# Kernel tuning notes

Hardware: AMD Instinct MI355X
Metric: run time of the kernel (lower is better)

Reference implementation:

```python
import jax, jax.numpy as jnp
import numpy as np

SEARCH_RANGE = 4  # matches args.search_range


def _displacements(r):
    # Exact channel ordering of the original double loop:
    # I=0 -> (0,0); then for i=1..r: (-i,0),(+i,0),(0,-i),(0,+i),
    # then for j=1..r: (-i,-j),(+i,+j),(-i,+j),(+i,-j).
    ds = [(0, 0)]
    for i in range(1, r + 1):
        ds += [(-i, 0), (i, 0), (0, -i), (0, i)]
        for j in range(1, r + 1):
            ds += [(-i, -j), (i, j), (-i, j), (i, -j)]
    return ds


def setup_inputs() -> dict:
    key = jax.random.key(0)
    k1, k2 = jax.random.split(key)
    B, C, H, W = 4, 128, 96, 160
    src = jax.random.normal(k1, (B, C, H, W), dtype=jnp.float32)
    tgt = jax.random.normal(k2, (B, C, H, W), dtype=jnp.float32)
    return {"src": src, "tgt": tgt}


def reference(src, tgt):
    r = SEARCH_RANGE
    B, C, H, W = src.shape
    D = (2 * r + 1) ** 2  # 81 displacement channels
    # Zero-pad tgt spatially so out-of-range shifted regions contribute 0,
    # matching the torch version's zero-initialized output slices.
    tgt_pad = jnp.pad(tgt, ((0, 0), (0, 0), (r, r), (r, r)))
    chans = []
    for dy, dx in _displacements(r):
        # shifted[b,c,y,x] = tgt[b,c,y+dy,x+dx] (0 outside)
        t = jax.lax.dynamic_slice(tgt_pad, (0, 0, r + dy, r + dx), (B, C, H, W))
        chans.append(jnp.einsum('bchw,bchw->bhw', src, t))
    out = jnp.stack(chans, axis=1)  # [B, D, H, W]
    return out / D
```

## Files before the change

kernel.cpp:

```cpp
#include <hip/hip_runtime.h>
#include <hip/hip_bf16.h>

#define BATCH 4
#define CHAN 128
#define HGT 96
#define WID 160
#define HW (HGT * WID)
#define THREADS 512

typedef __attribute__((ext_vector_type(8))) short short8;
typedef __attribute__((ext_vector_type(4))) float float4v;

__device__ __forceinline__ int chan_of(int dy, int dx) {
    if (dy == 0 && dx == 0) return 0;
    if (dx == 0) { int i = dy < 0 ? -dy : dy; return 1 + (i - 1) * 20 + (dy < 0 ? 0 : 1); }
    if (dy == 0) { int i = dx < 0 ? -dx : dx; return 1 + (i - 1) * 20 + (dx < 0 ? 2 : 3); }
    int i = dy < 0 ? -dy : dy;
    int j = dx < 0 ? -dx : dx;
    int s = (dy < 0) ? (dx < 0 ? 0 : 2) : (dx < 0 ? 3 : 1);
    return 1 + (i - 1) * 20 + 4 + (j - 1) * 4 + s;
}

__device__ __forceinline__ unsigned pk2(float a, float b) {
    __hip_bfloat162 h = __float22bfloat162_rn(make_float2(a, b));
    unsigned u;
    __builtin_memcpy(&u, &h, 4);
    return u;
}

union sl_u { uint4 v; short8 s; };

#define FST_DECODE(TAG, U)                                                    \
    const int u##TAG   = (U);                                                 \
    const int xq##TAG  = u##TAG % 6;                                          \
    const int r6##TAG  = u##TAG / 6;                              \
    const int oct##TAG = r6##TAG & 15;                                        \
    const int row##TAG = r6##TAG >> 4;                             \
    const int gr##TAG  = y0 - 4 + row##TAG;                                   \
    const int gx##TAG  = x0 - 4 + xq##TAG * 4;               \
    const bool ok##TAG = ((unsigned)gr##TAG < (unsigned)HGT) &&               \
                         ((unsigned)gx##TAG < (unsigned)WID);                 \
    const int ga##TAG  = tb + (oct##TAG * 8 * HGT + gr##TAG) * WID + gx##TAG;

#define FST_ISSUE(TAG, COND)                                                  \
    _Pragma("unroll")                                                         \
    for (int j = 0; j < 8; ++j)                                               \
        p##TAG[j] = (COND) ? *(const float4v*)(tgt + ga##TAG + j * HW)        \
                           : (float4v){0.f, 0.f, 0.f, 0.f};

#define FST_WRITE(TAG)                                                        \
    _Pragma("unroll")                                                         \
    for (int i = 0; i < 4; ++i) {                                             \
        const int xl = xq##TAG * 4 + i;                                       \
        uint4 val;                                                            \
        val.x = pk2(p##TAG[0][i], p##TAG[1][i]);                              \
        val.y = pk2(p##TAG[2][i], p##TAG[3][i]);                              \
        val.z = pk2(p##TAG[4][i], p##TAG[5][i]);                              \
        val.w = pk2(p##TAG[6][i], p##TAG[7][i]);                              \
        s_b[(row##TAG * 24 + xl) * 16 + (oct##TAG ^ (xl & 15))] = val;        \
    }

#define COMPUTE_DY(DD, DYI)                                                   \
    {                                                                         \
        const int rr = wvy + (DYI);                                           \
        float4v a0 = (float4v){0.f, 0.f, 0.f, 0.f};                           \
        float4v a1 = (float4v){0.f, 0.f, 0.f, 0.f};                           \
        _Pragma("unroll")                                                     \
        for (int ks = 0; ks < 4; ++ks) {                                      \
            sl_u b0;                                        \
            b0.v = s_b[(rr * 24 + ln) * 16 + ((q + ks * 4) ^ ln)];            \
            a0 = __builtin_amdgcn_mfma_f32_16x16x32_bf16(afr[ks], b0.s, a0, 0, 0, 0); \
        }                                                                     \
        _Pragma("unroll")                                                     \
        for (int ks = 0; ks < 4; ++ks) {                                      \
            sl_u b1;                                     \
            b1.v = s_b[(rr * 24 + 16 + ln) * 16 + ((q + ks * 4) ^ ln)];       \
            a1 = __builtin_amdgcn_mfma_f32_16x16x32_bf16(afr[ks], b1.s, a1, 0, 0, 0); \
        }                                                                     \
        aa0[DD] = a0; aa1[DD] = a1;                                           \
    }

#define EPI_DY(DD, DYI)                                                       \
    _Pragma("unroll")                                                         \
    for (int reg = 0; reg < 4; ++reg) {                                       \
        const int m = q * 4 + reg;                                            \
        const int t0x = ln - m;                            \
        if ((unsigned)t0x <= 8u)                                              \
            s_o[((DYI) * 9 + t0x) * 68 + wvy * 16 + m] = aa0[DD][reg] * inv;  \
        const int t1x = ln + 16 - m;                       \
        if ((unsigned)t1x <= 8u)                                              \
            s_o[((DYI) * 9 + t1x) * 68 + wvy * 16 + m] = aa1[DD][reg] * inv;  \
    }

__global__ __launch_bounds__(THREADS, 4)
void cost_volume_fused(const float* __restrict__ src,
                       const float* __restrict__ tgt,
                       float* __restrict__ out) {
    __shared__ __align__(16) uint4 s_b[4736];
    __shared__ int s_tab[81];

    const int tid  = threadIdx.x;
    const int wv   = tid >> 6;
    const int wvy  = wv & 3;
    const int wvd  = wv >> 2;
    const int lane = tid & 63;
    const int q    = lane >> 4;
    const int ln   = lane & 15;

    const int w    = blockIdx.x;
    const int slab = w & 7;
    const int b    = slab >> 1;
    const int yh   = slab & 1;
    const int t    = w >> 3;
    const int x0   = (t % 10) * 16;
    const int y0   = yh * 48 + (t / 10) * 4;

    if (tid < 81) s_tab[tid] = chan_of(tid / 9 - 4, tid % 9 - 4) * HW;

    const int tb = b * CHAN * HGT * WID;

    FST_DECODE(0, tid)
    FST_DECODE(1, tid + 512)
    FST_DECODE(2, tid + 1024)
    const bool has2 = tid < 128;

    float4v p0[8], p1[8], p2[8];

    FST_ISSUE(0, ok0)

    const int y = y0 + wvy;
    const int sbase = (b * CHAN * HGT + y) * WID + x0 + ln + q * 8 * HW;
    float apay[32];
    #pragma unroll
    for (int ks = 0; ks < 4; ++ks)
        #pragma unroll
        for (int j = 0; j < 8; ++j)
            apay[ks * 8 + j] = src[sbase + (ks * 32 + j) * HW];

    FST_ISSUE(1, ok1)
    FST_WRITE(0)
    FST_ISSUE(2, has2 && ok2)
    short8 afr[4];
    #pragma unroll
    for (int ks = 0; ks < 4; ++ks) {
        sl_u f;
        f.v.x = pk2(apay[ks * 8 + 0], apay[ks * 8 + 1]);
        f.v.y = pk2(apay[ks * 8 + 2], apay[ks * 8 + 3]);
        f.v.z = pk2(apay[ks * 8 + 4], apay[ks * 8 + 5]);
        f.v.w = pk2(apay[ks * 8 + 6], apay[ks * 8 + 7]);
        afr[ks] = f.s;
    }
    FST_WRITE(1)
    if (has2) { FST_WRITE(2) }

    __syncthreads();

    float4v aa0[5], aa1[5];
    if (wvd == 0) {
        #pragma unroll
        for (int dd = 0; dd < 4; ++dd) COMPUTE_DY(dd, dd)
    } else {
        #pragma unroll
        for (int dd = 0; dd < 5; ++dd) COMPUTE_DY(dd, dd + 4)
    }

    __syncthreads();

    float* s_o = (float*)s_b;
    const float inv = 1.0f / 81.0f;
    if (wvd == 0) {
        #pragma unroll
        for (int dd = 0; dd < 4; ++dd) EPI_DY(dd, dd)
    } else {
        #pragma unroll
        for (int dd = 0; dd < 5; ++dd) EPI_DY(dd, dd + 4)
    }
    __syncthreads();

    const size_t ob = (size_t)b * 81 * HW + (size_t)y0 * WID + x0;
    #pragma unroll
    for (int it = 0; it < 3; ++it) {
        const int v = it * THREADS + tid;
        if (v < 1296) {
            const int xq  = v & 3;
            const int row = v >> 2;
            const int cix = row >> 2;
            const int yy  = row & 3;
            float4v val = *(const float4v*)&s_o[cix * 68 + yy * 16 + xq * 4];
            *(float4v*)&out[ob + s_tab[cix] + yy * WID + xq * 4] = val;
        }
    }
}

extern "C" void kernel_launch(void* const* d_in, const int* in_sizes, int n_in,
                              void* d_out, int out_size, void* d_ws, size_t ws_size,
                              hipStream_t stream) {
    const float* src = (const float*)d_in[0];
    const float* tgt = (const float*)d_in[1];
    float* out = (float*)d_out;
    cost_volume_fused<<<dim3(960, 1, 1), dim3(THREADS, 1, 1), 0, stream>>>(src, tgt, out);
}
```

Measured before the change: 116.7 us.

## Pre-convert inputs to NHWC bf16 in a separate pass and load via LDS DMA

Adds a prepass kernel that transposes src and tgt from NCHW fp32 into NHWC bf16 in the workspace. The main MFMA kernel then loads tgt tiles straight into LDS with global_load_lds and reads src fragments as contiguous 16-byte vectors. This removes the strided per-channel fp32 loads and the in-register bf16 packing from the main kernel. In exchange it adds a second kernel launch and a full extra read and write of both inputs. The old fused kernel remains as a fallback when the workspace is too small.

```diff
diff --git a/kernel.cpp b/kernel.cpp
--- a/kernel.cpp
+++ b/kernel.cpp
@@ -7,6 +7,8 @@
 #define WID 160
 #define HW (HGT * WID)
 #define THREADS 512
+#define TENSOR_ELEMS (BATCH * CHAN * HGT * WID)
+#define WS_NEED ((size_t)(2 * (size_t)TENSOR_ELEMS * 2))
 
 typedef __attribute__((ext_vector_type(8))) short short8;
 typedef __attribute__((ext_vector_type(4))) float float4v;
@@ -30,14 +32,178 @@
 
 union sl_u { uint4 v; short8 s; };
 
+__global__ __launch_bounds__(256)
+void nhwc_bf16_kernel(const float* __restrict__ src,
+                      const float* __restrict__ tgt,
+                      ushort* __restrict__ ws) {
+    __shared__ unsigned s_t[64][65];
+    int r = blockIdx.x;
+    const int xb = r % 3; r /= 3;
+    const int y  = r % HGT; r /= HGT;
+    const int b  = r % BATCH; r /= BATCH;
+    const float* in = r ? tgt : src;
+    ushort* op0 = ws + (size_t)r * TENSOR_ELEMS;
+    const int x0 = xb * 64;
+    const int npx = (x0 + 64 <= WID) ? 64 : (WID - x0);
+
+    const int t  = threadIdx.x;
+    const int x1 = t & 63, cp0 = t >> 6;
+    if (x1 < npx) {
+        const int base = (b * CHAN * HGT + y) * WID + x0 + x1;
+        #pragma unroll
+        for (int i = 0; i < 16; ++i) {
+            const int cp = cp0 + i * 4;
+            s_t[cp][x1] = pk2(in[base + (2 * cp) * HW],
+                              in[base + (2 * cp + 1) * HW]);
+        }
+    }
+    __syncthreads();
+    const int x2 = t >> 2, g = t & 3;
+    if (x2 < npx) {
+        ushort* op = op0 + ((size_t)(b * HGT + y) * WID + x0 + x2) * CHAN + g * 32;
+        #pragma unroll
+        for (int k = 0; k < 4; ++k) {
+            uint4 v;
+            v.x = s_t[g * 16 + k * 4 + 0][x2];
+            v.y = s_t[g * 16 + k * 4 + 1][x2];
+            v.z = s_t[g * 16 + k * 4 + 2][x2];
+            v.w = s_t[g * 16 + k * 4 + 3][x2];
+            *(uint4*)(op + k * 8) = v;
+        }
+    }
+}
+
+__global__ __launch_bounds__(THREADS, 4)
+void cost_volume_mfma(const ushort* __restrict__ srcT,
+                      const ushort* __restrict__ tgtT,
+                      float* __restrict__ out) {
+    __shared__ __align__(16) uint4 s_b[4736];
+    __shared__ int s_tab[81];
+
+    const int tid  = threadIdx.x;
+    const int wv   = tid >> 6;
+    const int wvy  = wv & 3;
+    const int wvd  = wv >> 2;
+    const int lane = tid & 63;
+    const int q    = lane >> 4;
+    const int ln   = lane & 15;
+
+    const int w    = blockIdx.x;
+    const int slab = w & 7;
+    const int b    = slab >> 1;
+    const int yh   = slab & 1;
+    const int t    = w >> 3;
+    const int x0   = (t % 10) * 16;
+    const int y0   = yh * 48 + (t / 10) * 4;
+
+    if (tid < 81) s_tab[tid] = chan_of(tid / 9 - 4, tid % 9 - 4) * HW;
+
+    const ushort* tbase = tgtT + (size_t)b * HGT * WID * CHAN;
+    #pragma unroll
+    for (int k = 0; k < 9; ++k) {
+        const int u   = k * THREADS + tid;
+        const int j   = u & 15;
+        const int v16 = u >> 4;
+        const int row = v16 / 24;
+        const int x   = v16 - row * 24;
+        const int gr  = y0 - 4 + row;
+        const int gx  = x0 - 4 + x;
+        const int oct = j ^ (x & 15);
+        unsigned* lp = (unsigned*)&s_b[k * THREADS + (tid & ~63)];
+        if (((unsigned)gr < (unsigned)HGT) && ((unsigned)gx < (unsigned)WID)) {
+            const unsigned* gp =
+                (const unsigned*)(tbase + ((gr * WID + gx) * CHAN + oct * 8));
+            __builtin_amdgcn_global_load_lds(gp, lp, 16, 0, 0);
+        } else {
+            s_b[u] = make_uint4(0u, 0u, 0u, 0u);
+        }
+    }
+
+    const int y = y0 + wvy;
+    const ushort* abase =
+        srcT + ((size_t)(b * HGT + y) * WID + x0 + ln) * CHAN + q * 8;
+    short8 afr[4];
+    #pragma unroll
+    for (int ks = 0; ks < 4; ++ks)
+        afr[ks] = *(const short8*)(abase + ks * 32);
+
+    __syncthreads();
+
+    float4v aa0[5], aa1[5];
+    #define COMPUTE_DY(DD, DYI)                                               \
+        {                                                                     \
+            const int rr = wvy + (DYI);                                       \
+            float4v a0 = (float4v){0.f, 0.f, 0.f, 0.f};                       \
+            float4v a1 = (float4v){0.f, 0.f, 0.f, 0.f};                       \
+            _Pragma("unroll")                                                 \
+            for (int ks = 0; ks < 4; ++ks) {                                  \
+                sl_u b0;                                    \
+                b0.v = s_b[(rr * 24 + ln) * 16 + ((q + ks * 4) ^ ln)];        \
+                a0 = __builtin_amdgcn_mfma_f32_16x16x32_bf16(afr[ks], b0.s, a0, 0, 0, 0); \
+            }                                                                 \
+            _Pragma("unroll")                                                 \
+            for (int ks = 0; ks < 4; ++ks) {                                  \
+                sl_u b1;                                 \
+                b1.v = s_b[(rr * 24 + 16 + ln) * 16 + ((q + ks * 4) ^ ln)];   \
+                a1 = __builtin_amdgcn_mfma_f32_16x16x32_bf16(afr[ks], b1.s, a1, 0, 0, 0); \
+            }                                                                 \
+            aa0[DD] = a0; aa1[DD] = a1;                                       \
+        }
+    if (wvd == 0) {
+        #pragma unroll
+        for (int dd = 0; dd < 4; ++dd) COMPUTE_DY(dd, dd)
+    } else {
+        #pragma unroll
+        for (int dd = 0; dd < 5; ++dd) COMPUTE_DY(dd, dd + 4)
+    }
+
+    __syncthreads();
+
+    float* s_o = (float*)s_b;
+    const float inv = 1.0f / 81.0f;
+    #define EPI_DY(DD, DYI)                                                   \
+        _Pragma("unroll")                                                     \
+        for (int reg = 0; reg < 4; ++reg) {                                   \
+            const int m = q * 4 + reg;                                        \
+            const int t0x = ln - m;                        \
+            if ((unsigned)t0x <= 8u)                                          \
+                s_o[((DYI) * 9 + t0x) * 68 + wvy * 16 + m] = aa0[DD][reg] * inv; \
+            const int t1x = ln + 16 - m;                   \
+            if ((unsigned)t1x <= 8u)                                          \
+                s_o[((DYI) * 9 + t1x) * 68 + wvy * 16 + m] = aa1[DD][reg] * inv; \
+        }
+    if (wvd == 0) {
+        #pragma unroll
+        for (int dd = 0; dd < 4; ++dd) EPI_DY(dd, dd)
+    } else {
+        #pragma unroll
+        for (int dd = 0; dd < 5; ++dd) EPI_DY(dd, dd + 4)
+    }
+    __syncthreads();
+
+    const size_t ob = (size_t)b * 81 * HW + (size_t)y0 * WID + x0;
+    #pragma unroll
+    for (int it = 0; it < 3; ++it) {
+        const int v = it * THREADS + tid;
+        if (v < 1296) {
+            const int xq  = v & 3;
+            const int row = v >> 2;
+            const int cix = row >> 2;
+            const int yy  = row & 3;
+            float4v val = *(const float4v*)&s_o[cix * 68 + yy * 16 + xq * 4];
+            *(float4v*)&out[ob + s_tab[cix] + yy * WID + xq * 4] = val;
+        }
+    }
+}
+
 #define FST_DECODE(TAG, U)                                                    \
     const int u##TAG   = (U);                                                 \
     const int xq##TAG  = u##TAG % 6;                                          \
-    const int r6##TAG  = u##TAG / 6;                              \
+    const int r6##TAG  = u##TAG / 6;                                          \
     const int oct##TAG = r6##TAG & 15;                                        \
-    const int row##TAG = r6##TAG >> 4;                             \
+    const int row##TAG = r6##TAG >> 4;                                        \
     const int gr##TAG  = y0 - 4 + row##TAG;                                   \
-    const int gx##TAG  = x0 - 4 + xq##TAG * 4;               \
+    const int gx##TAG  = x0 - 4 + xq##TAG * 4;                                \
     const bool ok##TAG = ((unsigned)gr##TAG < (unsigned)HGT) &&               \
                          ((unsigned)gx##TAG < (unsigned)WID);                 \
     const int ga##TAG  = tb + (oct##TAG * 8 * HGT + gr##TAG) * WID + gx##TAG;
@@ -60,38 +226,6 @@
         s_b[(row##TAG * 24 + xl) * 16 + (oct##TAG ^ (xl & 15))] = val;        \
     }
 
-#define COMPUTE_DY(DD, DYI)                                                   \
-    {                                                                         \
-        const int rr = wvy + (DYI);                                           \
-        float4v a0 = (float4v){0.f, 0.f, 0.f, 0.f};                           \
-        float4v a1 = (float4v){0.f, 0.f, 0.f, 0.f};                           \
-        _Pragma("unroll")                                                     \
-        for (int ks = 0; ks < 4; ++ks) {                                      \
-            sl_u b0;                                        \
-            b0.v = s_b[(rr * 24 + ln) * 16 + ((q + ks * 4) ^ ln)];            \
-            a0 = __builtin_amdgcn_mfma_f32_16x16x32_bf16(afr[ks], b0.s, a0, 0, 0, 0); \
-        }                                                                     \
-        _Pragma("unroll")                                                     \
-        for (int ks = 0; ks < 4; ++ks) {                                      \
-            sl_u b1;                                     \
-            b1.v = s_b[(rr * 24 + 16 + ln) * 16 + ((q + ks * 4) ^ ln)];       \
-            a1 = __builtin_amdgcn_mfma_f32_16x16x32_bf16(afr[ks], b1.s, a1, 0, 0, 0); \
-        }                                                                     \
-        aa0[DD] = a0; aa1[DD] = a1;                                           \
-    }
-
-#define EPI_DY(DD, DYI)                                                       \
-    _Pragma("unroll")                                                         \
-    for (int reg = 0; reg < 4; ++reg) {                                       \
-        const int m = q * 4 + reg;                                            \
-        const int t0x = ln - m;                            \
-        if ((unsigned)t0x <= 8u)                                              \
-            s_o[((DYI) * 9 + t0x) * 68 + wvy * 16 + m] = aa0[DD][reg] * inv;  \
-        const int t1x = ln + 16 - m;                       \
-        if ((unsigned)t1x <= 8u)                                              \
-            s_o[((DYI) * 9 + t1x) * 68 + wvy * 16 + m] = aa1[DD][reg] * inv;  \
-    }
-
 __global__ __launch_bounds__(THREADS, 4)
 void cost_volume_fused(const float* __restrict__ src,
                        const float* __restrict__ tgt,
@@ -125,7 +259,6 @@
     const bool has2 = tid < 128;
 
     float4v p0[8], p1[8], p2[8];
-
     FST_ISSUE(0, ok0)
 
     const int y = y0 + wvy;
@@ -198,5 +331,12 @@
     const float* src = (const float*)d_in[0];
     const float* tgt = (const float*)d_in[1];
     float* out = (float*)d_out;
-    cost_volume_fused<<<dim3(960, 1, 1), dim3(THREADS, 1, 1), 0, stream>>>(src, tgt, out);
-}
+    if (d_ws && ws_size >= WS_NEED) {
+        ushort* ws = (ushort*)d_ws;
+        nhwc_bf16_kernel<<<dim3(2304, 1, 1), dim3(256, 1, 1), 0, stream>>>(src, tgt, ws);
+        cost_volume_mfma<<<dim3(960, 1, 1), dim3(THREADS, 1, 1), 0, stream>>>(
+            ws, ws + TENSOR_ELEMS, out);
+    } else {
+        cost_volume_fused<<<dim3(960, 1, 1), dim3(THREADS, 1, 1), 0, stream>>>(src, tgt, out);
+    }
+}
```

New measurement: 119.1 us. +2.0%, slower.
